# Performance work log

Measured on AMD Instinct MI355X. Metric: run time of the kernel, lower is better.

The kernel has to match this reference:

```python
import jax, jax.numpy as jnp
import numpy as np

LODS = [16, 32, 64, 128, 256]
SCENE_SCALE = 4.0
DESC = 4
N = 2_000_000
# 8 corner offsets of a voxel, bit-decoded: (x, y, z) in {0,1}^3
_CORNERS = jnp.asarray([[(i >> 2) & 1, (i >> 1) & 1, i & 1] for i in range(8)], dtype=jnp.int32)  # (8,3)


def setup_inputs() -> dict:
    key = jax.random.key(0)
    ks = jax.random.split(key, 2 + len(LODS))
    inp = {
        "pts": jax.random.normal(ks[0], (N, 3), dtype=jnp.float32),
        "d": jax.random.normal(ks[1], (N, 3), dtype=jnp.float32),
    }
    # codebook init mirrors torch: zeros + 0.01 * randn, shape (LOD^3, desc)
    for i, res in enumerate(LODS):
        inp[f"codebook_{i}"] = jax.random.normal(ks[2 + i], (res ** 3, DESC), dtype=jnp.float32) * 0.01
    return inp


def _trilerp(res, codebook, pts01):
    """NGLOD-style dense-grid trilinear interpolation.
    pts01: (N,3) in [0,1]; codebook: (res^3, DESC). Returns (N, DESC)."""
    pos = pts01 * (res - 1)                                   # (N,3) in [0, res-1]
    c0 = jnp.clip(jnp.floor(pos).astype(jnp.int32), 0, res - 2)
    frac = pos - c0.astype(pos.dtype)                         # (N,3) in [0,1]
    idx = c0[:, None, :] + _CORNERS[None, :, :]               # (N,8,3)
    flat = (idx[..., 0] * res + idx[..., 1]) * res + idx[..., 2]  # (N,8) row-major x*res^2+y*res+z
    # trilinear weights: prod over axes of (frac if corner bit set else 1-frac)
    w = jnp.prod(jnp.where(_CORNERS[None] == 1, frac[:, None, :], 1.0 - frac[:, None, :]), axis=-1)  # (N,8)
    return jnp.einsum('nkd,nk->nd', codebook[flat], w)        # gather + weighted sum


def reference(pts, d, codebook_0, codebook_1, codebook_2, codebook_3, codebook_4):
    cbs = (codebook_0, codebook_1, codebook_2, codebook_3, codebook_4)
    p = pts / SCENE_SCALE
    mask = jnp.all(jnp.abs(p) < 0.5, axis=-1)                 # inside unit cube
    p01 = jnp.clip(p + 0.5, 0.0, 1.0)                         # clamp keeps OOB points index-safe; masked out below
    feats = _trilerp(LODS[0], cbs[0], p01)
    for res, cb in zip(LODS[1:], cbs[1:]):
        feats = feats + _trilerp(res, cb, p01)                # sum features across LODs
    color = jnp.where(mask[:, None], feats[:, 0:3], 0.0)      # masked scatter into zero buffer
    log_sigma = jnp.where(mask, feats[:, 3], -100000.0)       # exp(-1e5) underflows to 0, as in torch
    return color, jnp.exp(log_sigma)[:, None]
```

## Files before the change

### kernel.cpp

```cpp
#include <hip/hip_runtime.h>
#include <math.h>

static constexpr float kSceneScale = 4.0f;
static constexpr int   kG     = 16;
static constexpr int   kNBins = kG * kG * kG + 1;
static constexpr int   kNB    = 256;

__device__ __forceinline__ void fma4(float4& acc, float w, const float4& c) {
    acc.x = fmaf(w, c.x, acc.x);
    acc.y = fmaf(w, c.y, acc.y);
    acc.z = fmaf(w, c.z, acc.z);
    acc.w = fmaf(w, c.w, acc.w);
}

template <int RES>
__device__ __forceinline__ void trilerp_acc(const float4* __restrict__ cb,
                                            float x, float y, float z,
                                            float4& acc) {
    const float s = (float)(RES - 1);
    float fx = x * s, fy = y * s, fz = z * s;
    int x0 = min((int)fx, RES - 2);
    int y0 = min((int)fy, RES - 2);
    int z0 = min((int)fz, RES - 2);
    float tx = fx - (float)x0;
    float ty = fy - (float)y0;
    float tz = fz - (float)z0;

    int base = (x0 * RES + y0) * RES + z0;

    float4 c000 = cb[base];
    float4 c001 = cb[base + 1];
    float4 c010 = cb[base + RES];
    float4 c011 = cb[base + RES + 1];
    float4 c100 = cb[base + RES * RES];
    float4 c101 = cb[base + RES * RES + 1];
    float4 c110 = cb[base + RES * RES + RES];
    float4 c111 = cb[base + RES * RES + RES + 1];

    float wx0 = 1.0f - tx, wx1 = tx;
    float wy0 = 1.0f - ty, wy1 = ty;
    float wz0 = 1.0f - tz, wz1 = tz;

    fma4(acc, wx0 * wy0 * wz0, c000);
    fma4(acc, wx0 * wy0 * wz1, c001);
    fma4(acc, wx0 * wy1 * wz0, c010);
    fma4(acc, wx0 * wy1 * wz1, c011);
    fma4(acc, wx1 * wy0 * wz0, c100);
    fma4(acc, wx1 * wy0 * wz1, c101);
    fma4(acc, wx1 * wy1 * wz0, c110);
    fma4(acc, wx1 * wy1 * wz1, c111);
}

__device__ __forceinline__ void load_p01(const float* __restrict__ pts, int i,
                                         float& x, float& y, float& z, bool& inside) {
    float px = pts[3 * i + 0] * (1.0f / kSceneScale);
    float py = pts[3 * i + 1] * (1.0f / kSceneScale);
    float pz = pts[3 * i + 2] * (1.0f / kSceneScale);
    inside = (fabsf(px) < 0.5f) && (fabsf(py) < 0.5f) && (fabsf(pz) < 0.5f);
    x = fminf(fmaxf(px + 0.5f, 0.0f), 1.0f);
    y = fminf(fmaxf(py + 0.5f, 0.0f), 1.0f);
    z = fminf(fmaxf(pz + 0.5f, 0.0f), 1.0f);
}

__device__ __forceinline__ unsigned point_key(const float* __restrict__ pts, int i) {
    float x, y, z; bool inside;
    load_p01(pts, i, x, y, z, inside);
    if (!inside) return (unsigned)(kNBins - 1);
    int bx = min((int)(x * kG), kG - 1);
    int by = min((int)(y * kG), kG - 1);
    int bz = min((int)(z * kG), kG - 1);
    return (unsigned)((bx * kG + by) * kG + bz);
}

__global__ __launch_bounds__(256) void keys_hist_kernel(
        const float* __restrict__ pts, unsigned* __restrict__ keys,
        unsigned* __restrict__ blockHist, int n, int chunk) {
    __shared__ unsigned hist[kNBins];
    int tid = threadIdx.x;
    for (int j = tid; j < kNBins; j += 256) hist[j] = 0;
    __syncthreads();
    int beg = blockIdx.x * chunk;
    int end = min(n, beg + chunk);
    for (int i = beg + tid; i < end; i += 256) {
        unsigned key = point_key(pts, i);
        keys[i] = key;
        atomicAdd(&hist[key], 1u);
    }
    __syncthreads();
    for (int j = tid; j < kNBins; j += 256) blockHist[(size_t)j * kNB + blockIdx.x] = hist[j];
}

__global__ __launch_bounds__(256) void scan_chunks_kernel(
        unsigned* __restrict__ data, unsigned* __restrict__ partials, int total) {
    __shared__ unsigned sums[256];
    int tid = threadIdx.x;
    int base = blockIdx.x * 1024 + tid * 4;
    uint4 v = make_uint4(0u, 0u, 0u, 0u);
    if (base + 3 < total) {
        v = *(const uint4*)(data + base);
    } else {
        unsigned* p = (unsigned*)&v;
        for (int k = 0; k < 4; ++k) if (base + k < total) p[k] = data[base + k];
    }
    unsigned s1 = v.x + v.y, s2 = s1 + v.z, s3 = s2 + v.w;
    sums[tid] = s3;
    __syncthreads();
    for (int off = 1; off < 256; off <<= 1) {
        unsigned t = (tid >= off) ? sums[tid - off] : 0u;
        __syncthreads();
        sums[tid] += t;
        __syncthreads();
    }
    unsigned excl = sums[tid] - s3;
    uint4 o;
    o.x = excl; o.y = excl + v.x; o.z = excl + s1; o.w = excl + s2;
    if (base + 3 < total) {
        *(uint4*)(data + base) = o;
    } else {
        unsigned* p = (unsigned*)&o;
        for (int k = 0; k < 4; ++k) if (base + k < total) data[base + k] = p[k];
    }
    if (tid == 255) partials[blockIdx.x] = sums[255];
}

__global__ __launch_bounds__(256) void scan_partials_kernel(unsigned* __restrict__ partials, int m) {
    __shared__ unsigned buf[256];
    __shared__ unsigned carry_s;
    int tid = threadIdx.x;
    if (tid == 0) carry_s = 0u;
    __syncthreads();
    for (int base = 0; base < m; base += 256) {
        unsigned v = (base + tid < m) ? partials[base + tid] : 0u;
        buf[tid] = v;
        __syncthreads();
        for (int off = 1; off < 256; off <<= 1) {
            unsigned t = (tid >= off) ? buf[tid - off] : 0u;
            __syncthreads();
            buf[tid] += t;
            __syncthreads();
        }
        unsigned incl = buf[tid];
        unsigned c = carry_s;
        if (base + tid < m) partials[base + tid] = c + incl - v;
        __syncthreads();
        if (tid == 255) carry_s = c + incl;
        __syncthreads();
    }
}

__global__ __launch_bounds__(256) void scan_add_kernel(
        unsigned* __restrict__ data, const unsigned* __restrict__ partials, int total) {
    int tid = threadIdx.x;
    int base = blockIdx.x * 1024 + tid * 4;
    unsigned p = partials[blockIdx.x];
    if (base + 3 < total) {
        uint4 v = *(const uint4*)(data + base);
        v.x += p; v.y += p; v.z += p; v.w += p;
        *(uint4*)(data + base) = v;
    } else {
        for (int k = 0; k < 4; ++k) if (base + k < total) data[base + k] += p;
    }
}

__global__ __launch_bounds__(256) void scatter_kernel(
        const unsigned* __restrict__ keys, const unsigned* __restrict__ blockHist,
        unsigned* __restrict__ order, int n, int chunk) {
    __shared__ unsigned offs[kNBins];
    int tid = threadIdx.x;
    for (int j = tid; j < kNBins; j += 256) offs[j] = blockHist[(size_t)j * kNB + blockIdx.x];
    __syncthreads();
    int beg = blockIdx.x * chunk;
    int end = min(n, beg + chunk);
    for (int i = beg + tid; i < end; i += 256) {
        unsigned k = keys[i];
        unsigned pos = atomicAdd(&offs[k], 1u);
        order[pos] = (unsigned)i;
    }
}

__global__ __launch_bounds__(256) void compute_kernel(
        const float* __restrict__ pts,
        const unsigned* __restrict__ order,
        const float4* __restrict__ cb0,
        const float4* __restrict__ cb1,
        const float4* __restrict__ cb2,
        const float4* __restrict__ cb3,
        const float4* __restrict__ cb4,
        float* __restrict__ out,
        int n) {
    int t = blockIdx.x * blockDim.x + threadIdx.x;
    if (t >= n) return;
    int i = (int)order[t];

    float x, y, z; bool inside;
    load_p01(pts, i, x, y, z, inside);

    float c0 = 0.0f, c1 = 0.0f, c2 = 0.0f, sg = 0.0f;
    if (inside) {
        float4 acc = make_float4(0.0f, 0.0f, 0.0f, 0.0f);
        trilerp_acc<16>(cb0, x, y, z, acc);
        trilerp_acc<32>(cb1, x, y, z, acc);
        trilerp_acc<64>(cb2, x, y, z, acc);
        trilerp_acc<128>(cb3, x, y, z, acc);
        trilerp_acc<256>(cb4, x, y, z, acc);
        c0 = acc.x; c1 = acc.y; c2 = acc.z; sg = expf(acc.w);
    }

    out[3 * i + 0] = c0;
    out[3 * i + 1] = c1;
    out[3 * i + 2] = c2;
    out[(size_t)3 * n + i] = sg;
}

__global__ __launch_bounds__(256) void direct_kernel(
        const float* __restrict__ pts,
        const float4* __restrict__ cb0,
        const float4* __restrict__ cb1,
        const float4* __restrict__ cb2,
        const float4* __restrict__ cb3,
        const float4* __restrict__ cb4,
        float* __restrict__ out,
        int n) {
    int i = blockIdx.x * blockDim.x + threadIdx.x;
    if (i >= n) return;
    float x, y, z; bool inside;
    load_p01(pts, i, x, y, z, inside);
    float c0 = 0.0f, c1 = 0.0f, c2 = 0.0f, sg = 0.0f;
    if (inside) {
        float4 acc = make_float4(0.0f, 0.0f, 0.0f, 0.0f);
        trilerp_acc<16>(cb0, x, y, z, acc);
        trilerp_acc<32>(cb1, x, y, z, acc);
        trilerp_acc<64>(cb2, x, y, z, acc);
        trilerp_acc<128>(cb3, x, y, z, acc);
        trilerp_acc<256>(cb4, x, y, z, acc);
        c0 = acc.x; c1 = acc.y; c2 = acc.z; sg = expf(acc.w);
    }
    out[3 * i + 0] = c0;
    out[3 * i + 1] = c1;
    out[3 * i + 2] = c2;
    out[(size_t)3 * n + i] = sg;
}

extern "C" void kernel_launch(void* const* d_in, const int* in_sizes, int n_in,
                              void* d_out, int out_size, void* d_ws, size_t ws_size,
                              hipStream_t stream) {
    const float* pts = (const float*)d_in[0];
    const float4* cb0 = (const float4*)d_in[2];
    const float4* cb1 = (const float4*)d_in[3];
    const float4* cb2 = (const float4*)d_in[4];
    const float4* cb3 = (const float4*)d_in[5];
    const float4* cb4 = (const float4*)d_in[6];
    float* out = (float*)d_out;

    int n = in_sizes[0] / 3;

    const int histTotal = kNBins * kNB;
    const int nChunks   = (histTotal + 1023) / 1024;

    size_t off_keys  = 0;
    size_t off_order = off_keys + (size_t)n * 4;
    size_t off_hist  = off_order + (size_t)n * 4;
    size_t off_part  = off_hist + (size_t)histTotal * 4;
    size_t need      = off_part + (size_t)nChunks * 4;

    dim3 block(256);
    dim3 gridN((n + 255) / 256);

    if (ws_size < need) {
        direct_kernel<<<gridN, block, 0, stream>>>(pts, cb0, cb1, cb2, cb3, cb4, out, n);
        return;
    }

    unsigned* keys      = (unsigned*)((char*)d_ws + off_keys);
    unsigned* order     = (unsigned*)((char*)d_ws + off_order);
    unsigned* blockHist = (unsigned*)((char*)d_ws + off_hist);
    unsigned* partials  = (unsigned*)((char*)d_ws + off_part);

    int chunk = (n + kNB - 1) / kNB;

    keys_hist_kernel<<<dim3(kNB), block, 0, stream>>>(pts, keys, blockHist, n, chunk);
    scan_chunks_kernel<<<dim3(nChunks), block, 0, stream>>>(blockHist, partials, histTotal);
    scan_partials_kernel<<<dim3(1), block, 0, stream>>>(partials, nChunks);
    scan_add_kernel<<<dim3(nChunks), block, 0, stream>>>(blockHist, partials, histTotal);
    scatter_kernel<<<dim3(kNB), block, 0, stream>>>(keys, blockHist, order, n, chunk);
    compute_kernel<<<gridN, block, 0, stream>>>(pts, order, cb0, cb1, cb2, cb3, cb4, out, n);
}
```

Measured before the change: 288.1 us.

## Gather finest codebook in bf16, pre-sort packed points, swizzle blocks across XCDs

```diff
diff --git a/kernel.cpp b/kernel.cpp
--- a/kernel.cpp
+++ b/kernel.cpp
@@ -5,6 +5,8 @@
 static constexpr int   kG     = 16;
 static constexpr int   kNBins = kG * kG * kG + 1;
 static constexpr int   kNB    = 256;
+static constexpr int   kRes4  = 256;
+static constexpr int   kCells4 = kRes4 * kRes4 * kRes4;
 
 __device__ __forceinline__ void fma4(float4& acc, float w, const float4& c) {
     acc.x = fmaf(w, c.x, acc.x);
@@ -49,6 +51,53 @@
     fma4(acc, wx1 * wy0 * wz1, c101);
     fma4(acc, wx1 * wy1 * wz0, c110);
     fma4(acc, wx1 * wy1 * wz1, c111);
+}
+
+__device__ __forceinline__ float4 bfdec(uint2 w) {
+    float4 r;
+    r.x = __uint_as_float(w.x << 16);
+    r.y = __uint_as_float(w.x & 0xFFFF0000u);
+    r.z = __uint_as_float(w.y << 16);
+    r.w = __uint_as_float(w.y & 0xFFFF0000u);
+    return r;
+}
+
+template <int RES>
+__device__ __forceinline__ void trilerp_bf16(const uint2* __restrict__ cb,
+                                             float x, float y, float z,
+                                             float4& acc) {
+    const float s = (float)(RES - 1);
+    float fx = x * s, fy = y * s, fz = z * s;
+    int x0 = min((int)fx, RES - 2);
+    int y0 = min((int)fy, RES - 2);
+    int z0 = min((int)fz, RES - 2);
+    float tx = fx - (float)x0;
+    float ty = fy - (float)y0;
+    float tz = fz - (float)z0;
+
+    int base = (x0 * RES + y0) * RES + z0;
+
+    uint2 w000 = cb[base];
+    uint2 w001 = cb[base + 1];
+    uint2 w010 = cb[base + RES];
+    uint2 w011 = cb[base + RES + 1];
+    uint2 w100 = cb[base + RES * RES];
+    uint2 w101 = cb[base + RES * RES + 1];
+    uint2 w110 = cb[base + RES * RES + RES];
+    uint2 w111 = cb[base + RES * RES + RES + 1];
+
+    float wx0 = 1.0f - tx, wx1 = tx;
+    float wy0 = 1.0f - ty, wy1 = ty;
+    float wz0 = 1.0f - tz, wz1 = tz;
+
+    fma4(acc, wx0 * wy0 * wz0, bfdec(w000));
+    fma4(acc, wx0 * wy0 * wz1, bfdec(w001));
+    fma4(acc, wx0 * wy1 * wz0, bfdec(w010));
+    fma4(acc, wx0 * wy1 * wz1, bfdec(w011));
+    fma4(acc, wx1 * wy0 * wz0, bfdec(w100));
+    fma4(acc, wx1 * wy0 * wz1, bfdec(w101));
+    fma4(acc, wx1 * wy1 * wz0, bfdec(w110));
+    fma4(acc, wx1 * wy1 * wz1, bfdec(w111));
 }
 
 __device__ __forceinline__ void load_p01(const float* __restrict__ pts, int i,
@@ -163,8 +212,9 @@
 }
 
 __global__ __launch_bounds__(256) void scatter_kernel(
+        const float* __restrict__ pts,
         const unsigned* __restrict__ keys, const unsigned* __restrict__ blockHist,
-        unsigned* __restrict__ order, int n, int chunk) {
+        float4* __restrict__ spts, int n, int chunk) {
     __shared__ unsigned offs[kNBins];
     int tid = threadIdx.x;
     for (int j = tid; j < kNBins; j += 256) offs[j] = blockHist[(size_t)j * kNB + blockIdx.x];
@@ -173,39 +223,98 @@
     int end = min(n, beg + chunk);
     for (int i = beg + tid; i < end; i += 256) {
         unsigned k = keys[i];
+        float x, y, z; bool inside;
+        load_p01(pts, i, x, y, z, inside);
         unsigned pos = atomicAdd(&offs[k], 1u);
-        order[pos] = (unsigned)i;
-    }
-}
-
-__global__ __launch_bounds__(256) void compute_kernel(
-        const float* __restrict__ pts,
-        const unsigned* __restrict__ order,
+        unsigned tag = (unsigned)i | (inside ? 0x80000000u : 0u);
+        spts[pos] = make_float4(x, y, z, __uint_as_float(tag));
+    }
+}
+
+__device__ __forceinline__ unsigned bf16r(float f) {
+    unsigned u = __float_as_uint(f);
+    return (u + 0x7FFFu + ((u >> 16) & 1u)) >> 16;
+}
+__device__ __forceinline__ unsigned pk2(float lo, float hi) {
+    return bf16r(lo) | (bf16r(hi) << 16);
+}
+__global__ __launch_bounds__(256) void convert_cb4_kernel(
+        const float4* __restrict__ src, uint4* __restrict__ dst, int npairs) {
+    int t = blockIdx.x * blockDim.x + threadIdx.x;
+    if (t >= npairs) return;
+    float4 a = src[2 * t];
+    float4 b = src[2 * t + 1];
+    dst[t] = make_uint4(pk2(a.x, a.y), pk2(a.z, a.w), pk2(b.x, b.y), pk2(b.z, b.w));
+}
+
+__device__ __forceinline__ int xcd_swz(int orig, int nwg) {
+    const int NX = 8;
+    int q = nwg / NX, r = nwg % NX;
+    int xcd = orig % NX, j = orig / NX;
+    int base = (xcd < r) ? xcd * (q + 1) : r * (q + 1) + (xcd - r) * q;
+    return base + j;
+}
+
+__global__ __launch_bounds__(256) void compute_bf16_kernel(
+        const float4* __restrict__ spts,
+        const float4* __restrict__ cb0,
+        const float4* __restrict__ cb1,
+        const float4* __restrict__ cb2,
+        const float4* __restrict__ cb3,
+        const uint2*  __restrict__ cb4b,
+        float* __restrict__ out,
+        int n, int nwg) {
+    int bid = xcd_swz(blockIdx.x, nwg);
+    int t = bid * blockDim.x + threadIdx.x;
+    if (t >= n) return;
+    float4 s = spts[t];
+    unsigned tag = __float_as_uint(s.w);
+    bool inside = (tag & 0x80000000u) != 0u;
+    int i = (int)(tag & 0x7FFFFFFFu);
+
+    float c0 = 0.0f, c1 = 0.0f, c2 = 0.0f, sg = 0.0f;
+    if (inside) {
+        float4 acc = make_float4(0.0f, 0.0f, 0.0f, 0.0f);
+        trilerp_acc<16>(cb0, s.x, s.y, s.z, acc);
+        trilerp_acc<32>(cb1, s.x, s.y, s.z, acc);
+        trilerp_acc<64>(cb2, s.x, s.y, s.z, acc);
+        trilerp_acc<128>(cb3, s.x, s.y, s.z, acc);
+        trilerp_bf16<256>(cb4b, s.x, s.y, s.z, acc);
+        c0 = acc.x; c1 = acc.y; c2 = acc.z; sg = expf(acc.w);
+    }
+    out[3 * i + 0] = c0;
+    out[3 * i + 1] = c1;
+    out[3 * i + 2] = c2;
+    out[(size_t)3 * n + i] = sg;
+}
+
+__global__ __launch_bounds__(256) void compute_fp32_kernel(
+        const float4* __restrict__ spts,
         const float4* __restrict__ cb0,
         const float4* __restrict__ cb1,
         const float4* __restrict__ cb2,
         const float4* __restrict__ cb3,
         const float4* __restrict__ cb4,
         float* __restrict__ out,
-        int n) {
-    int t = blockIdx.x * blockDim.x + threadIdx.x;
+        int n, int nwg) {
+    int bid = xcd_swz(blockIdx.x, nwg);
+    int t = bid * blockDim.x + threadIdx.x;
     if (t >= n) return;
-    int i = (int)order[t];
-
-    float x, y, z; bool inside;
-    load_p01(pts, i, x, y, z, inside);
+    float4 s = spts[t];
+    unsigned tag = __float_as_uint(s.w);
+    bool inside = (tag & 0x80000000u) != 0u;
+    int i = (int)(tag & 0x7FFFFFFFu);
 
     float c0 = 0.0f, c1 = 0.0f, c2 = 0.0f, sg = 0.0f;
     if (inside) {
         float4 acc = make_float4(0.0f, 0.0f, 0.0f, 0.0f);
-        trilerp_acc<16>(cb0, x, y, z, acc);
-        trilerp_acc<32>(cb1, x, y, z, acc);
-        trilerp_acc<64>(cb2, x, y, z, acc);
-        trilerp_acc<128>(cb3, x, y, z, acc);
-        trilerp_acc<256>(cb4, x, y, z, acc);
+        trilerp_acc<16>(cb0, s.x, s.y, s.z, acc);
+        trilerp_acc<32>(cb1, s.x, s.y, s.z, acc);
+        trilerp_acc<64>(cb2, s.x, s.y, s.z, acc);
+        trilerp_acc<128>(cb3, s.x, s.y, s.z, acc);
+        trilerp_acc<256>(cb4, s.x, s.y, s.z, acc);
         c0 = acc.x; c1 = acc.y; c2 = acc.z; sg = expf(acc.w);
     }
-
     out[3 * i + 0] = c0;
     out[3 * i + 1] = c1;
     out[3 * i + 2] = c2;
@@ -257,24 +366,27 @@
     const int histTotal = kNBins * kNB;
     const int nChunks   = (histTotal + 1023) / 1024;
 
-    size_t off_keys  = 0;
-    size_t off_order = off_keys + (size_t)n * 4;
-    size_t off_hist  = off_order + (size_t)n * 4;
-    size_t off_part  = off_hist + (size_t)histTotal * 4;
-    size_t need      = off_part + (size_t)nChunks * 4;
+    size_t off_keys = 0;
+    size_t off_spts = (off_keys + (size_t)n * 4 + 15) & ~(size_t)15;
+    size_t off_hist = off_spts + (size_t)n * 16;
+    size_t off_part = off_hist + (size_t)histTotal * 4;
+    size_t off_cb4b = (off_part + (size_t)nChunks * 4 + 255) & ~(size_t)255;
+    size_t need_sort = off_part + (size_t)nChunks * 4;
+    size_t need_bf16 = off_cb4b + (size_t)kCells4 * 8;
 
     dim3 block(256);
-    dim3 gridN((n + 255) / 256);
-
-    if (ws_size < need) {
-        direct_kernel<<<gridN, block, 0, stream>>>(pts, cb0, cb1, cb2, cb3, cb4, out, n);
+    int nwg = (n + 255) / 256;
+
+    if (ws_size < need_sort) {
+        direct_kernel<<<dim3(nwg), block, 0, stream>>>(pts, cb0, cb1, cb2, cb3, cb4, out, n);
         return;
     }
 
     unsigned* keys      = (unsigned*)((char*)d_ws + off_keys);
-    unsigned* order     = (unsigned*)((char*)d_ws + off_order);
+    float4*   spts      = (float4*)((char*)d_ws + off_spts);
     unsigned* blockHist = (unsigned*)((char*)d_ws + off_hist);
     unsigned* partials  = (unsigned*)((char*)d_ws + off_part);
+    uint2*    cb4b      = (uint2*)((char*)d_ws + off_cb4b);
 
     int chunk = (n + kNB - 1) / kNB;
 
@@ -282,6 +394,15 @@
     scan_chunks_kernel<<<dim3(nChunks), block, 0, stream>>>(blockHist, partials, histTotal);
     scan_partials_kernel<<<dim3(1), block, 0, stream>>>(partials, nChunks);
     scan_add_kernel<<<dim3(nChunks), block, 0, stream>>>(blockHist, partials, histTotal);
-    scatter_kernel<<<dim3(kNB), block, 0, stream>>>(keys, blockHist, order, n, chunk);
-    compute_kernel<<<gridN, block, 0, stream>>>(pts, order, cb0, cb1, cb2, cb3, cb4, out, n);
-}
+    scatter_kernel<<<dim3(kNB), block, 0, stream>>>(pts, keys, blockHist, spts, n, chunk);
+
+    if (ws_size >= need_bf16) {
+        const int npairs = kCells4 / 2;
+        convert_cb4_kernel<<<dim3(npairs / 256), block, 0, stream>>>(cb4, (uint4*)cb4b, npairs);
+        compute_bf16_kernel<<<dim3(nwg), block, 0, stream>>>(
+            spts, cb0, cb1, cb2, cb3, (const uint2*)cb4b, out, n, nwg);
+    } else {
+        compute_fp32_kernel<<<dim3(nwg), block, 0, stream>>>(
+            spts, cb0, cb1, cb2, cb3, cb4, out, n, nwg);
+    }
+}
```

Result: slower. 370.4 us (+28.6%).

## Stage per-bin codebook tiles in LDS and fuse point packing into scatter

Applied to the files above, without the earlier changes.

```diff
diff --git a/kernel.cpp b/kernel.cpp
--- a/kernel.cpp
+++ b/kernel.cpp
@@ -5,12 +5,35 @@
 static constexpr int   kG     = 16;
 static constexpr int   kNBins = kG * kG * kG + 1;
 static constexpr int   kNB    = 256;
+static constexpr int   kDirectThresh = 48;
+
+static constexpr int kS4 = 18;
+static constexpr int kS3 = 10;
+static constexpr int kS2 = 6;
+static constexpr int kS1 = 4;
+static constexpr int kS0 = 3;
 
 __device__ __forceinline__ void fma4(float4& acc, float w, const float4& c) {
     acc.x = fmaf(w, c.x, acc.x);
     acc.y = fmaf(w, c.y, acc.y);
     acc.z = fmaf(w, c.z, acc.z);
     acc.w = fmaf(w, c.w, acc.w);
+}
+
+__device__ __forceinline__ unsigned bf16r(float f) {
+    unsigned u = __float_as_uint(f);
+    return (u + 0x7FFFu + ((u >> 16) & 1u)) >> 16;
+}
+__device__ __forceinline__ unsigned pk2(float lo, float hi) {
+    return bf16r(lo) | (bf16r(hi) << 16);
+}
+__device__ __forceinline__ float4 bfdec(uint2 w) {
+    float4 r;
+    r.x = __uint_as_float(w.x << 16);
+    r.y = __uint_as_float(w.x & 0xFFFF0000u);
+    r.z = __uint_as_float(w.y << 16);
+    r.w = __uint_as_float(w.y & 0xFFFF0000u);
+    return r;
 }
 
 template <int RES>
@@ -25,9 +48,7 @@
     float tx = fx - (float)x0;
     float ty = fy - (float)y0;
     float tz = fz - (float)z0;
-
     int base = (x0 * RES + y0) * RES + z0;
-
     float4 c000 = cb[base];
     float4 c001 = cb[base + 1];
     float4 c010 = cb[base + RES];
@@ -36,11 +57,9 @@
     float4 c101 = cb[base + RES * RES + 1];
     float4 c110 = cb[base + RES * RES + RES];
     float4 c111 = cb[base + RES * RES + RES + 1];
-
     float wx0 = 1.0f - tx, wx1 = tx;
     float wy0 = 1.0f - ty, wy1 = ty;
     float wz0 = 1.0f - tz, wz1 = tz;
-
     fma4(acc, wx0 * wy0 * wz0, c000);
     fma4(acc, wx0 * wy0 * wz1, c001);
     fma4(acc, wx0 * wy1 * wz0, c010);
@@ -163,8 +182,9 @@
 }
 
 __global__ __launch_bounds__(256) void scatter_kernel(
+        const float* __restrict__ pts,
         const unsigned* __restrict__ keys, const unsigned* __restrict__ blockHist,
-        unsigned* __restrict__ order, int n, int chunk) {
+        float4* __restrict__ spts, float* __restrict__ out, int n, int chunk) {
     __shared__ unsigned offs[kNBins];
     int tid = threadIdx.x;
     for (int j = tid; j < kNBins; j += 256) offs[j] = blockHist[(size_t)j * kNB + blockIdx.x];
@@ -173,14 +193,120 @@
     int end = min(n, beg + chunk);
     for (int i = beg + tid; i < end; i += 256) {
         unsigned k = keys[i];
+        float x, y, z; bool inside;
+        load_p01(pts, i, x, y, z, inside);
         unsigned pos = atomicAdd(&offs[k], 1u);
-        order[pos] = (unsigned)i;
-    }
-}
-
-__global__ __launch_bounds__(256) void compute_kernel(
-        const float* __restrict__ pts,
-        const unsigned* __restrict__ order,
+        if (inside) {
+            spts[pos] = make_float4(x, y, z, __uint_as_float((unsigned)i));
+        } else {
+            out[3 * i + 0] = 0.0f;
+            out[3 * i + 1] = 0.0f;
+            out[3 * i + 2] = 0.0f;
+            out[(size_t)3 * n + i] = 0.0f;
+        }
+    }
+}
+
+template <int RES, int SPAN>
+__device__ __forceinline__ void stage_bf16(const float4* __restrict__ cb, uint2* sbuf,
+                                           int lox, int loy, int loz, int tid, int nthr) {
+    for (int c = tid; c < SPAN * SPAN * SPAN; c += nthr) {
+        int cz = c % SPAN;
+        int cy = (c / SPAN) % SPAN;
+        int cx = c / (SPAN * SPAN);
+        int gx = min(lox + cx, RES - 1);
+        int gy = min(loy + cy, RES - 1);
+        int gz = min(loz + cz, RES - 1);
+        float4 v = cb[((size_t)gx * RES + gy) * RES + gz];
+        sbuf[c] = make_uint2(pk2(v.x, v.y), pk2(v.z, v.w));
+    }
+}
+
+template <int RES, int SPAN>
+__device__ __forceinline__ void stage_f32(const float4* __restrict__ cb, float4* sbuf,
+                                          int lox, int loy, int loz, int tid, int nthr) {
+    for (int c = tid; c < SPAN * SPAN * SPAN; c += nthr) {
+        int cz = c % SPAN;
+        int cy = (c / SPAN) % SPAN;
+        int cx = c / (SPAN * SPAN);
+        int gx = min(lox + cx, RES - 1);
+        int gy = min(loy + cy, RES - 1);
+        int gz = min(loz + cz, RES - 1);
+        sbuf[c] = cb[((size_t)gx * RES + gy) * RES + gz];
+    }
+}
+
+template <int RES, int SPAN>
+__device__ __forceinline__ void lerp_lds_bf16(const uint2* sbuf,
+                                              int lox, int loy, int loz,
+                                              float x, float y, float z, float4& acc) {
+    const float s = (float)(RES - 1);
+    float fx = x * s, fy = y * s, fz = z * s;
+    int x0 = min((int)fx, RES - 2);
+    int y0 = min((int)fy, RES - 2);
+    int z0 = min((int)fz, RES - 2);
+    float tx = fx - (float)x0;
+    float ty = fy - (float)y0;
+    float tz = fz - (float)z0;
+    int base = ((x0 - lox) * SPAN + (y0 - loy)) * SPAN + (z0 - loz);
+    uint2 w000 = sbuf[base];
+    uint2 w001 = sbuf[base + 1];
+    uint2 w010 = sbuf[base + SPAN];
+    uint2 w011 = sbuf[base + SPAN + 1];
+    uint2 w100 = sbuf[base + SPAN * SPAN];
+    uint2 w101 = sbuf[base + SPAN * SPAN + 1];
+    uint2 w110 = sbuf[base + SPAN * SPAN + SPAN];
+    uint2 w111 = sbuf[base + SPAN * SPAN + SPAN + 1];
+    float wx0 = 1.0f - tx, wx1 = tx;
+    float wy0 = 1.0f - ty, wy1 = ty;
+    float wz0 = 1.0f - tz, wz1 = tz;
+    fma4(acc, wx0 * wy0 * wz0, bfdec(w000));
+    fma4(acc, wx0 * wy0 * wz1, bfdec(w001));
+    fma4(acc, wx0 * wy1 * wz0, bfdec(w010));
+    fma4(acc, wx0 * wy1 * wz1, bfdec(w011));
+    fma4(acc, wx1 * wy0 * wz0, bfdec(w100));
+    fma4(acc, wx1 * wy0 * wz1, bfdec(w101));
+    fma4(acc, wx1 * wy1 * wz0, bfdec(w110));
+    fma4(acc, wx1 * wy1 * wz1, bfdec(w111));
+}
+
+template <int RES, int SPAN>
+__device__ __forceinline__ void lerp_lds_f32(const float4* sbuf,
+                                             int lox, int loy, int loz,
+                                             float x, float y, float z, float4& acc) {
+    const float s = (float)(RES - 1);
+    float fx = x * s, fy = y * s, fz = z * s;
+    int x0 = min((int)fx, RES - 2);
+    int y0 = min((int)fy, RES - 2);
+    int z0 = min((int)fz, RES - 2);
+    float tx = fx - (float)x0;
+    float ty = fy - (float)y0;
+    float tz = fz - (float)z0;
+    int base = ((x0 - lox) * SPAN + (y0 - loy)) * SPAN + (z0 - loz);
+    float4 c000 = sbuf[base];
+    float4 c001 = sbuf[base + 1];
+    float4 c010 = sbuf[base + SPAN];
+    float4 c011 = sbuf[base + SPAN + 1];
+    float4 c100 = sbuf[base + SPAN * SPAN];
+    float4 c101 = sbuf[base + SPAN * SPAN + 1];
+    float4 c110 = sbuf[base + SPAN * SPAN + SPAN];
+    float4 c111 = sbuf[base + SPAN * SPAN + SPAN + 1];
+    float wx0 = 1.0f - tx, wx1 = tx;
+    float wy0 = 1.0f - ty, wy1 = ty;
+    float wz0 = 1.0f - tz, wz1 = tz;
+    fma4(acc, wx0 * wy0 * wz0, c000);
+    fma4(acc, wx0 * wy0 * wz1, c001);
+    fma4(acc, wx0 * wy1 * wz0, c010);
+    fma4(acc, wx0 * wy1 * wz1, c011);
+    fma4(acc, wx1 * wy0 * wz0, c100);
+    fma4(acc, wx1 * wy0 * wz1, c101);
+    fma4(acc, wx1 * wy1 * wz0, c110);
+    fma4(acc, wx1 * wy1 * wz1, c111);
+}
+
+__global__ __launch_bounds__(512) void compute_tiled_kernel(
+        const float4* __restrict__ spts,
+        const unsigned* __restrict__ blockHist,
         const float4* __restrict__ cb0,
         const float4* __restrict__ cb1,
         const float4* __restrict__ cb2,
@@ -188,28 +314,65 @@
         const float4* __restrict__ cb4,
         float* __restrict__ out,
         int n) {
-    int t = blockIdx.x * blockDim.x + threadIdx.x;
-    if (t >= n) return;
-    int i = (int)order[t];
-
-    float x, y, z; bool inside;
-    load_p01(pts, i, x, y, z, inside);
-
-    float c0 = 0.0f, c1 = 0.0f, c2 = 0.0f, sg = 0.0f;
-    if (inside) {
+    int bin = blockIdx.x;
+    unsigned start = blockHist[(size_t)bin * kNB];
+    unsigned end   = blockHist[(size_t)(bin + 1) * kNB];
+    if (start >= end) return;
+
+    int bx = bin >> 8, by = (bin >> 4) & 15, bz = bin & 15;
+    int tid = threadIdx.x;
+
+    if ((int)(end - start) < kDirectThresh) {
+        for (unsigned t = start + tid; t < end; t += 512) {
+            float4 s = spts[t];
+            int i = (int)__float_as_uint(s.w);
+            float4 acc = make_float4(0.0f, 0.0f, 0.0f, 0.0f);
+            trilerp_acc<16>(cb0, s.x, s.y, s.z, acc);
+            trilerp_acc<32>(cb1, s.x, s.y, s.z, acc);
+            trilerp_acc<64>(cb2, s.x, s.y, s.z, acc);
+            trilerp_acc<128>(cb3, s.x, s.y, s.z, acc);
+            trilerp_acc<256>(cb4, s.x, s.y, s.z, acc);
+            out[3 * i + 0] = acc.x;
+            out[3 * i + 1] = acc.y;
+            out[3 * i + 2] = acc.z;
+            out[(size_t)3 * n + i] = expf(acc.w);
+        }
+        return;
+    }
+
+    __shared__ uint2  s4[kS4 * kS4 * kS4];
+    __shared__ uint2  s3[kS3 * kS3 * kS3];
+    __shared__ float4 s2[kS2 * kS2 * kS2];
+    __shared__ float4 s1[kS1 * kS1 * kS1];
+    __shared__ float4 s0[kS0 * kS0 * kS0];
+
+    int lox4 = (bx * 255) >> 4, loy4 = (by * 255) >> 4, loz4 = (bz * 255) >> 4;
+    int lox3 = (bx * 127) >> 4, loy3 = (by * 127) >> 4, loz3 = (bz * 127) >> 4;
+    int lox2 = (bx * 63) >> 4,  loy2 = (by * 63) >> 4,  loz2 = (bz * 63) >> 4;
+    int lox1 = (bx * 31) >> 4,  loy1 = (by * 31) >> 4,  loz1 = (bz * 31) >> 4;
+    int lox0 = (bx * 15) >> 4,  loy0 = (by * 15) >> 4,  loz0 = (bz * 15) >> 4;
+
+    stage_bf16<256, kS4>(cb4, s4, lox4, loy4, loz4, tid, 512);
+    stage_bf16<128, kS3>(cb3, s3, lox3, loy3, loz3, tid, 512);
+    stage_f32<64,  kS2>(cb2, s2, lox2, loy2, loz2, tid, 512);
+    stage_f32<32,  kS1>(cb1, s1, lox1, loy1, loz1, tid, 512);
+    stage_f32<16,  kS0>(cb0, s0, lox0, loy0, loz0, tid, 512);
+    __syncthreads();
+
+    for (unsigned t = start + tid; t < end; t += 512) {
+        float4 s = spts[t];
+        int i = (int)__float_as_uint(s.w);
         float4 acc = make_float4(0.0f, 0.0f, 0.0f, 0.0f);
-        trilerp_acc<16>(cb0, x, y, z, acc);
-        trilerp_acc<32>(cb1, x, y, z, acc);
-        trilerp_acc<64>(cb2, x, y, z, acc);
-        trilerp_acc<128>(cb3, x, y, z, acc);
-        trilerp_acc<256>(cb4, x, y, z, acc);
-        c0 = acc.x; c1 = acc.y; c2 = acc.z; sg = expf(acc.w);
-    }
-
-    out[3 * i + 0] = c0;
-    out[3 * i + 1] = c1;
-    out[3 * i + 2] = c2;
-    out[(size_t)3 * n + i] = sg;
+        lerp_lds_f32<16,  kS0>(s0, lox0, loy0, loz0, s.x, s.y, s.z, acc);
+        lerp_lds_f32<32,  kS1>(s1, lox1, loy1, loz1, s.x, s.y, s.z, acc);
+        lerp_lds_f32<64,  kS2>(s2, lox2, loy2, loz2, s.x, s.y, s.z, acc);
+        lerp_lds_bf16<128, kS3>(s3, lox3, loy3, loz3, s.x, s.y, s.z, acc);
+        lerp_lds_bf16<256, kS4>(s4, lox4, loy4, loz4, s.x, s.y, s.z, acc);
+        out[3 * i + 0] = acc.x;
+        out[3 * i + 1] = acc.y;
+        out[3 * i + 2] = acc.z;
+        out[(size_t)3 * n + i] = expf(acc.w);
+    }
 }
 
 __global__ __launch_bounds__(256) void direct_kernel(
@@ -257,22 +420,22 @@
     const int histTotal = kNBins * kNB;
     const int nChunks   = (histTotal + 1023) / 1024;
 
-    size_t off_keys  = 0;
-    size_t off_order = off_keys + (size_t)n * 4;
-    size_t off_hist  = off_order + (size_t)n * 4;
-    size_t off_part  = off_hist + (size_t)histTotal * 4;
-    size_t need      = off_part + (size_t)nChunks * 4;
+    size_t off_keys = 0;
+    size_t off_spts = (off_keys + (size_t)n * 4 + 15) & ~(size_t)15;
+    size_t off_hist = off_spts + (size_t)n * 16;
+    size_t off_part = off_hist + (size_t)histTotal * 4;
+    size_t need     = off_part + (size_t)nChunks * 4;
 
     dim3 block(256);
-    dim3 gridN((n + 255) / 256);
+    int nwg = (n + 255) / 256;
 
     if (ws_size < need) {
-        direct_kernel<<<gridN, block, 0, stream>>>(pts, cb0, cb1, cb2, cb3, cb4, out, n);
+        direct_kernel<<<dim3(nwg), block, 0, stream>>>(pts, cb0, cb1, cb2, cb3, cb4, out, n);
         return;
     }
 
     unsigned* keys      = (unsigned*)((char*)d_ws + off_keys);
-    unsigned* order     = (unsigned*)((char*)d_ws + off_order);
+    float4*   spts      = (float4*)((char*)d_ws + off_spts);
     unsigned* blockHist = (unsigned*)((char*)d_ws + off_hist);
     unsigned* partials  = (unsigned*)((char*)d_ws + off_part);
 
@@ -282,6 +445,7 @@
     scan_chunks_kernel<<<dim3(nChunks), block, 0, stream>>>(blockHist, partials, histTotal);
     scan_partials_kernel<<<dim3(1), block, 0, stream>>>(partials, nChunks);
     scan_add_kernel<<<dim3(nChunks), block, 0, stream>>>(blockHist, partials, histTotal);
-    scatter_kernel<<<dim3(kNB), block, 0, stream>>>(keys, blockHist, order, n, chunk);
-    compute_kernel<<<gridN, block, 0, stream>>>(pts, order, cb0, cb1, cb2, cb3, cb4, out, n);
-}
+    scatter_kernel<<<dim3(kNB), block, 0, stream>>>(pts, keys, blockHist, spts, out, n, chunk);
+    compute_tiled_kernel<<<dim3(kG * kG * kG), dim3(512), 0, stream>>>(
+        spts, blockHist, cb0, cb1, cb2, cb3, cb4, out, n);
+}
```

After: 320.7 us. +11.3%, slower.

## Scatter sorted inside points, compute contiguously with two points per thread, then unsort

Applied to the files above, without the earlier changes.

```diff
diff --git a/kernel.cpp b/kernel.cpp
--- a/kernel.cpp
+++ b/kernel.cpp
@@ -3,8 +3,10 @@
 
 static constexpr float kSceneScale = 4.0f;
 static constexpr int   kG     = 16;
-static constexpr int   kNBins = kG * kG * kG + 1;
+static constexpr int   kNBin3 = kG * kG * kG;
+static constexpr int   kNBins = kNBin3 + 1;
 static constexpr int   kNB    = 256;
+static constexpr unsigned kOutside = 0xFFFFFFFFu;
 
 __device__ __forceinline__ void fma4(float4& acc, float w, const float4& c) {
     acc.x = fmaf(w, c.x, acc.x);
@@ -25,9 +27,7 @@
     float tx = fx - (float)x0;
     float ty = fy - (float)y0;
     float tz = fz - (float)z0;
-
     int base = (x0 * RES + y0) * RES + z0;
-
     float4 c000 = cb[base];
     float4 c001 = cb[base + 1];
     float4 c010 = cb[base + RES];
@@ -36,11 +36,9 @@
     float4 c101 = cb[base + RES * RES + 1];
     float4 c110 = cb[base + RES * RES + RES];
     float4 c111 = cb[base + RES * RES + RES + 1];
-
     float wx0 = 1.0f - tx, wx1 = tx;
     float wy0 = 1.0f - ty, wy1 = ty;
     float wz0 = 1.0f - tz, wz1 = tz;
-
     fma4(acc, wx0 * wy0 * wz0, c000);
     fma4(acc, wx0 * wy0 * wz1, c001);
     fma4(acc, wx0 * wy1 * wz0, c010);
@@ -62,9 +60,7 @@
     z = fminf(fmaxf(pz + 0.5f, 0.0f), 1.0f);
 }
 
-__device__ __forceinline__ unsigned point_key(const float* __restrict__ pts, int i) {
-    float x, y, z; bool inside;
-    load_p01(pts, i, x, y, z, inside);
+__device__ __forceinline__ unsigned key_from01(float x, float y, float z, bool inside) {
     if (!inside) return (unsigned)(kNBins - 1);
     int bx = min((int)(x * kG), kG - 1);
     int by = min((int)(y * kG), kG - 1);
@@ -73,7 +69,7 @@
 }
 
 __global__ __launch_bounds__(256) void keys_hist_kernel(
-        const float* __restrict__ pts, unsigned* __restrict__ keys,
+        const float* __restrict__ pts,
         unsigned* __restrict__ blockHist, int n, int chunk) {
     __shared__ unsigned hist[kNBins];
     int tid = threadIdx.x;
@@ -82,9 +78,9 @@
     int beg = blockIdx.x * chunk;
     int end = min(n, beg + chunk);
     for (int i = beg + tid; i < end; i += 256) {
-        unsigned key = point_key(pts, i);
-        keys[i] = key;
-        atomicAdd(&hist[key], 1u);
+        float x, y, z; bool inside;
+        load_p01(pts, i, x, y, z, inside);
+        atomicAdd(&hist[key_from01(x, y, z, inside)], 1u);
     }
     __syncthreads();
     for (int j = tid; j < kNBins; j += 256) blockHist[(size_t)j * kNB + blockIdx.x] = hist[j];
@@ -163,8 +159,10 @@
 }
 
 __global__ __launch_bounds__(256) void scatter_kernel(
-        const unsigned* __restrict__ keys, const unsigned* __restrict__ blockHist,
-        unsigned* __restrict__ order, int n, int chunk) {
+        const float* __restrict__ pts,
+        const unsigned* __restrict__ blockHist,
+        float4* __restrict__ spts, unsigned* __restrict__ inv,
+        int n, int chunk) {
     __shared__ unsigned offs[kNBins];
     int tid = threadIdx.x;
     for (int j = tid; j < kNBins; j += 256) offs[j] = blockHist[(size_t)j * kNB + blockIdx.x];
@@ -172,44 +170,70 @@
     int beg = blockIdx.x * chunk;
     int end = min(n, beg + chunk);
     for (int i = beg + tid; i < end; i += 256) {
-        unsigned k = keys[i];
+        float x, y, z; bool inside;
+        load_p01(pts, i, x, y, z, inside);
+        unsigned k = key_from01(x, y, z, inside);
         unsigned pos = atomicAdd(&offs[k], 1u);
-        order[pos] = (unsigned)i;
-    }
-}
-
-__global__ __launch_bounds__(256) void compute_kernel(
-        const float* __restrict__ pts,
-        const unsigned* __restrict__ order,
+        if (inside) {
+            spts[pos] = make_float4(x, y, z, 0.0f);
+            inv[i] = pos;
+        } else {
+            inv[i] = kOutside;
+        }
+    }
+}
+
+__global__ __launch_bounds__(512) void compute_sorted_kernel(
+        const float4* __restrict__ spts,
+        const unsigned* __restrict__ nInsidePtr,
         const float4* __restrict__ cb0,
         const float4* __restrict__ cb1,
         const float4* __restrict__ cb2,
         const float4* __restrict__ cb3,
         const float4* __restrict__ cb4,
-        float* __restrict__ out,
-        int n) {
-    int t = blockIdx.x * blockDim.x + threadIdx.x;
-    if (t >= n) return;
-    int i = (int)order[t];
-
-    float x, y, z; bool inside;
-    load_p01(pts, i, x, y, z, inside);
-
-    float c0 = 0.0f, c1 = 0.0f, c2 = 0.0f, sg = 0.0f;
-    if (inside) {
-        float4 acc = make_float4(0.0f, 0.0f, 0.0f, 0.0f);
-        trilerp_acc<16>(cb0, x, y, z, acc);
-        trilerp_acc<32>(cb1, x, y, z, acc);
-        trilerp_acc<64>(cb2, x, y, z, acc);
-        trilerp_acc<128>(cb3, x, y, z, acc);
-        trilerp_acc<256>(cb4, x, y, z, acc);
-        c0 = acc.x; c1 = acc.y; c2 = acc.z; sg = expf(acc.w);
-    }
-
-    out[3 * i + 0] = c0;
-    out[3 * i + 1] = c1;
-    out[3 * i + 2] = c2;
-    out[(size_t)3 * n + i] = sg;
+        float4* __restrict__ sout) {
+    unsigned nIn = nInsidePtr[0];
+    unsigned t0 = blockIdx.x * 1024u + threadIdx.x;
+    unsigned t1 = t0 + 512u;
+    if (t0 >= nIn) return;
+
+    float4 sA = spts[t0];
+    bool doB = (t1 < nIn);
+    float4 sB = doB ? spts[t1] : sA;
+
+    float4 accA = make_float4(0.0f, 0.0f, 0.0f, 0.0f);
+    float4 accB = make_float4(0.0f, 0.0f, 0.0f, 0.0f);
+
+    trilerp_acc<16>(cb0, sA.x, sA.y, sA.z, accA);
+    trilerp_acc<16>(cb1 - 0 + 0, sB.x, sB.y, sB.z, accB);
+    accB = make_float4(0.0f, 0.0f, 0.0f, 0.0f);
+    trilerp_acc<16>(cb0, sB.x, sB.y, sB.z, accB);
+    trilerp_acc<32>(cb1, sA.x, sA.y, sA.z, accA);
+    trilerp_acc<32>(cb1, sB.x, sB.y, sB.z, accB);
+    trilerp_acc<64>(cb2, sA.x, sA.y, sA.z, accA);
+    trilerp_acc<64>(cb2, sB.x, sB.y, sB.z, accB);
+    trilerp_acc<128>(cb3, sA.x, sA.y, sA.z, accA);
+    trilerp_acc<128>(cb3, sB.x, sB.y, sB.z, accB);
+    trilerp_acc<256>(cb4, sA.x, sA.y, sA.z, accA);
+    trilerp_acc<256>(cb4, sB.x, sB.y, sB.z, accB);
+
+    sout[t0] = make_float4(accA.x, accA.y, accA.z, expf(accA.w));
+    if (doB) sout[t1] = make_float4(accB.x, accB.y, accB.z, expf(accB.w));
+}
+
+__global__ __launch_bounds__(256) void unsort_kernel(
+        const unsigned* __restrict__ inv,
+        const float4* __restrict__ sout,
+        float* __restrict__ out, int n) {
+    int i = blockIdx.x * blockDim.x + threadIdx.x;
+    if (i >= n) return;
+    unsigned v = inv[i];
+    float4 r = make_float4(0.0f, 0.0f, 0.0f, 0.0f);
+    if (v != kOutside) r = sout[v];
+    out[3 * i + 0] = r.x;
+    out[3 * i + 1] = r.y;
+    out[3 * i + 2] = r.z;
+    out[(size_t)3 * n + i] = r.w;
 }
 
 __global__ __launch_bounds__(256) void direct_kernel(
@@ -257,31 +281,37 @@
     const int histTotal = kNBins * kNB;
     const int nChunks   = (histTotal + 1023) / 1024;
 
-    size_t off_keys  = 0;
-    size_t off_order = off_keys + (size_t)n * 4;
-    size_t off_hist  = off_order + (size_t)n * 4;
-    size_t off_part  = off_hist + (size_t)histTotal * 4;
-    size_t need      = off_part + (size_t)nChunks * 4;
+    size_t off_spts = 0;
+    size_t off_sout = off_spts + (size_t)n * 16;
+    size_t off_hist = off_sout + (size_t)n * 16;
+    size_t off_part = off_hist + (size_t)histTotal * 4;
+    size_t off_inv  = off_part + (size_t)nChunks * 4;
+    size_t need     = off_inv + (size_t)n * 4;
 
     dim3 block(256);
-    dim3 gridN((n + 255) / 256);
+    int nwg = (n + 255) / 256;
 
     if (ws_size < need) {
-        direct_kernel<<<gridN, block, 0, stream>>>(pts, cb0, cb1, cb2, cb3, cb4, out, n);
+        direct_kernel<<<dim3(nwg), block, 0, stream>>>(pts, cb0, cb1, cb2, cb3, cb4, out, n);
         return;
     }
 
-    unsigned* keys      = (unsigned*)((char*)d_ws + off_keys);
-    unsigned* order     = (unsigned*)((char*)d_ws + off_order);
+    float4*   spts      = (float4*)((char*)d_ws + off_spts);
+    float4*   sout      = (float4*)((char*)d_ws + off_sout);
     unsigned* blockHist = (unsigned*)((char*)d_ws + off_hist);
     unsigned* partials  = (unsigned*)((char*)d_ws + off_part);
+    unsigned* inv       = (unsigned*)((char*)d_ws + off_inv);
+
+    const unsigned* nInsidePtr = blockHist + (size_t)kNBin3 * kNB;
 
     int chunk = (n + kNB - 1) / kNB;
 
-    keys_hist_kernel<<<dim3(kNB), block, 0, stream>>>(pts, keys, blockHist, n, chunk);
+    keys_hist_kernel<<<dim3(kNB), block, 0, stream>>>(pts, blockHist, n, chunk);
     scan_chunks_kernel<<<dim3(nChunks), block, 0, stream>>>(blockHist, partials, histTotal);
     scan_partials_kernel<<<dim3(1), block, 0, stream>>>(partials, nChunks);
     scan_add_kernel<<<dim3(nChunks), block, 0, stream>>>(blockHist, partials, histTotal);
-    scatter_kernel<<<dim3(kNB), block, 0, stream>>>(keys, blockHist, order, n, chunk);
-    compute_kernel<<<gridN, block, 0, stream>>>(pts, order, cb0, cb1, cb2, cb3, cb4, out, n);
-}
+    scatter_kernel<<<dim3(kNB), block, 0, stream>>>(pts, blockHist, spts, inv, n, chunk);
+    compute_sorted_kernel<<<dim3((n + 1023) / 1024), dim3(512), 0, stream>>>(
+        spts, nInsidePtr, cb0, cb1, cb2, cb3, cb4, sout);
+    unsort_kernel<<<dim3(nwg), block, 0, stream>>>(inv, sout, out, n);
+}
```

New measurement: 271.3 us. 1.06x faster.
